# Performance work log

Measured on AMD Instinct MI355X. Metric: run time of the kernel, lower is better.

The kernel has to match this reference:

```python
import jax, jax.numpy as jnp
import numpy as np

BLOCK = 64
SCALING = 64 / 64  # alpha / block_size


def setup_inputs() -> dict:
    key = jax.random.key(0)
    ks = jax.random.split(key, 5)
    B, N, DIN, DOUT = 2, 2048, 4096, 4096
    nb_in, nb_out = DIN // BLOCK, DOUT // BLOCK
    return {
        "x": jax.random.normal(ks[0], (B, N, DIN), dtype=jnp.float32),
        "W_base": jax.random.normal(ks[1], (DOUT, DIN), dtype=jnp.float32) * 0.02,
        "b_base": jax.random.normal(ks[2], (DOUT,), dtype=jnp.float32),
        "U": jax.random.normal(ks[3], (BLOCK, nb_in, nb_out), dtype=jnp.float32) / BLOCK,
        "V": jax.random.normal(ks[4], (nb_out, BLOCK, BLOCK), dtype=jnp.float32) * 0.02,
        "S": jnp.ones((1,), dtype=jnp.float32),
    }


def reference(x, W_base, b_base, U, V, S):
    B, N, DIN = x.shape
    DOUT = W_base.shape[0]
    nb_in = U.shape[1]  # in_features // block_size
    # base linear: y = x @ W^T + b
    result = jnp.einsum("bnd,od->bno", x, W_base) + b_base
    # block-structured adapter path
    xr = x.reshape(B, N, nb_in, BLOCK)            # [b, n, in_blocks, block]
    t = jnp.einsum("bnid,dio->bnod", xr, U)       # mix across input blocks per lane d
    t = jnp.einsum("bnod,ode->bnoe", t, V)        # mix within each output block
    scaling = SCALING * S[0]
    result = result + scaling * t.reshape(B, N, DOUT)
    return result
```

## Files before the change

kernel.cpp:

```cpp
#include <hip/hip_runtime.h>


typedef __attribute__((ext_vector_type(4))) float float4v;
typedef __attribute__((ext_vector_type(4))) int   int4v;
typedef __attribute__((ext_vector_type(2))) int   int2v;

#define K_TOT 4096
#define M_TOT 4096
#define N_TOT 4096

__global__ void trans_uv(const float* __restrict__ U, const float* __restrict__ V,
                         float* __restrict__ Ut, float* __restrict__ Vt) {
  int idx = blockIdx.x * 256 + threadIdx.x;
  if (idx < 262144) {
    int d = idx & 63, o = (idx >> 6) & 63, i = idx >> 12;
    Ut[idx] = U[(d * 64 + i) * 64 + o];
  } else {
    int j = idx - 262144;
    int d = j & 63, e = (j >> 6) & 63, o = j >> 12;
    Vt[j] = V[(o * 64 + d) * 64 + e];
  }
}

__global__ __launch_bounds__(512) void quant_rows(
    const float* __restrict__ W, const float* __restrict__ Ut,
    const float* __restrict__ Vt, const float* __restrict__ Sp,
    const float* __restrict__ X, char* __restrict__ Wq, char* __restrict__ Xq,
    float* __restrict__ sw, float* __restrict__ sx) {
  __shared__ float red[8];
  const int row = blockIdx.x;
  const int t = threadIdx.x;
  const int c0 = t << 3;
  const float s = Sp[0];
  float4v v0, v1;
  if (row < 4096) {
    const int o = row >> 6, e = row & 63;
    const int i = c0 >> 6, d0 = c0 & 63;
    const float4v wv0 = *(const float4v*)(W + (size_t)row * 4096 + c0);
    const float4v wv1 = *(const float4v*)(W + (size_t)row * 4096 + c0 + 4);
    const float4v u40 = *(const float4v*)(Ut + (i * 64 + o) * 64 + d0);
    const float4v u41 = *(const float4v*)(Ut + (i * 64 + o) * 64 + d0 + 4);
    const float4v v40 = *(const float4v*)(Vt + (o * 64 + e) * 64 + d0);
    const float4v v41 = *(const float4v*)(Vt + (o * 64 + e) * 64 + d0 + 4);
#pragma unroll
    for (int j = 0; j < 4; ++j) {
      v0[j] = wv0[j] + s * u40[j] * v40[j];
      v1[j] = wv1[j] + s * u41[j] * v41[j];
    }
  } else {
    v0 = *(const float4v*)(X + (size_t)(row - 4096) * 4096 + c0);
    v1 = *(const float4v*)(X + (size_t)(row - 4096) * 4096 + c0 + 4);
  }
  float m = fmaxf(fmaxf(fmaxf(fabsf(v0[0]), fabsf(v0[1])),
                        fmaxf(fabsf(v0[2]), fabsf(v0[3]))),
                  fmaxf(fmaxf(fabsf(v1[0]), fabsf(v1[1])),
                        fmaxf(fabsf(v1[2]), fabsf(v1[3]))));
#pragma unroll
  for (int off = 32; off; off >>= 1) m = fmaxf(m, __shfl_xor(m, off));
  if ((t & 63) == 0) red[t >> 6] = m;
  __syncthreads();
  float mx = red[0];
#pragma unroll
  for (int r = 1; r < 8; ++r) mx = fmaxf(mx, red[r]);
  const float inv = mx > 0.f ? 127.f / mx : 0.f;
  int q[8];
#pragma unroll
  for (int j = 0; j < 4; ++j) {
    int a = __float2int_rn(v0[j] * inv);
    int b2 = __float2int_rn(v1[j] * inv);
    q[j] = a > 127 ? 127 : (a < -127 ? -127 : a);
    q[4 + j] = b2 > 127 ? 127 : (b2 < -127 ? -127 : b2);
  }
  int2v pk;
  pk[0] = (q[0] & 0xff) | ((q[1] & 0xff) << 8) | ((q[2] & 0xff) << 16) |
          (q[3] << 24);
  pk[1] = (q[4] & 0xff) | ((q[5] & 0xff) << 8) | ((q[6] & 0xff) << 16) |
          (q[7] << 24);
  if (row < 4096) {
    *(int2v*)(Wq + (size_t)row * 4096 + c0) = pk;
    if (t == 0) sw[row] = mx * (1.f / 127.f);
  } else {
    *(int2v*)(Xq + (size_t)(row - 4096) * 4096 + c0) = pk;
    if (t == 0) sx[row - 4096] = mx * (1.f / 127.f);
  }
}

#define GL16(g, l)                                                    \
  __builtin_amdgcn_global_load_lds(                                   \
      (__attribute__((address_space(1))) void*)(g),                   \
      (__attribute__((address_space(3))) void*)(l), 16, 0, 0)

#define BARRIER() asm volatile("s_barrier" ::: "memory")
#define VMC6() asm volatile("s_waitcnt vmcnt(6)" ::: "memory")
#define VMC0() asm volatile("s_waitcnt vmcnt(0)" ::: "memory")
#define VMNONE()

__global__ __launch_bounds__(512, 2) void gemm256(
    const char* __restrict__ A,
    const char* __restrict__ Bq,
    const float* __restrict__ bias,
    const float* __restrict__ sx,
    const float* __restrict__ sw,
    float* __restrict__ C) {
  __shared__ char lds[2][2][2][16384];

  const int tid = threadIdx.x;
  const int w = tid >> 6;
  const int l = tid & 63;
  const int l15 = l & 15;
  const int hi = l >> 4;

  int b = blockIdx.x;
  b = (b & 7) * 32 + (b >> 3);
  const int brow = (b >> 4) * 256;
  const int bcol = (b & 15) * 256;

  const int wr = w >> 2;
  const int wc = w & 3;
  const int wcH = wc >> 1, wcL = wc & 1;

  const int b2 = (l15 >> 2) & 1;
  const int cx = hi ^ (l15 & 3);
  const int rdK0 = (((b2 ^ 0) << 2) | cx) << 4;
  const int rdK1 = (((b2 ^ 1) << 2) | cx) << 4;
  const int rowOff = l15 << 7;

  const int rowL = l >> 3;
  const int cL = (l & 7) ^ rowL;
  const char* pa = A + (size_t)(brow + w * 8 + rowL) * 4096 + cL * 16;
  const char* pb = Bq + (size_t)(bcol + w * 8 + rowL) * 4096 + cL * 16;
  const int ldsC0 = w * 1024;
  const int ldsC1 = 8192 + w * 1024;

#define STAGE(gp, BUF, OP, H, kt)                                           \
  do {                                                                      \
    GL16((gp) + (size_t)(H) * (128 * 4096) + (kt), &lds[BUF][OP][H][ldsC0]);\
    GL16((gp) + (size_t)(H) * (128 * 4096) + (64 * 4096) + (kt),            \
         &lds[BUF][OP][H][ldsC1]);                                          \
  } while (0)

  int4v acc[8][4];
#pragma unroll
  for (int m = 0; m < 8; ++m)
#pragma unroll
    for (int j = 0; j < 4; ++j) acc[m][j] = (int4v){0, 0, 0, 0};
  int4v af[4][2];
  int4v bfr[4][2];

#define READ_A(BUF, MB)                                                     \
  _Pragma("unroll") for (int mm = 0; mm < 4; ++mm) {                        \
    const char* ap = &lds[BUF][0][wr][((MB) + mm) * 2048 + rowOff];         \
    af[mm][0] = *(const int4v*)&ap[rdK0];                                   \
    af[mm][1] = *(const int4v*)&ap[rdK1];                                   \
  }

#define READ_B(BUF, NH)                                                     \
  _Pragma("unroll") for (int jj = 0; jj < 2; ++jj) {                        \
    const char* bp =                                                        \
        &lds[BUF][1][wcH][((wcL)*64 + (NH)*32 + jj * 16) * 128 + rowOff];   \
    bfr[(NH)*2 + jj][0] = *(const int4v*)&bp[rdK0];                         \
    bfr[(NH)*2 + jj][1] = *(const int4v*)&bp[rdK1];                         \
  }

#define MFMA16(MB, NB)                                                      \
  do {                                                                      \
    __builtin_amdgcn_s_setprio(1);                                          \
    _Pragma("unroll") for (int mm = 0; mm < 4; ++mm)                        \
        _Pragma("unroll") for (int nn = 0; nn < 2; ++nn) {                  \
      acc[(MB) + mm][(NB) + nn] = __builtin_amdgcn_mfma_i32_16x16x64_i8(    \
          af[mm][0], bfr[(NB) + nn][0], acc[(MB) + mm][(NB) + nn], 0, 0, 0);\
      acc[(MB) + mm][(NB) + nn] = __builtin_amdgcn_mfma_i32_16x16x64_i8(    \
          af[mm][1], bfr[(NB) + nn][1], acc[(MB) + mm][(NB) + nn], 0, 0, 0);\
    }                                                                       \
    __builtin_amdgcn_s_setprio(0);                                          \
  } while (0)

#define TILE(BUF, TT, DA1, DB, DA0, VM)                                    \
  do {                                                                     \
    READ_A(BUF, 0); READ_B(BUF, 0);                                        \
    if (DA1) STAGE(pa, 1 - (BUF), 0, 1, ((TT) + 1) * 128);                 \
    BARRIER(); MFMA16(0, 0);                                               \
    READ_B(BUF, 1);                                                        \
    BARRIER(); MFMA16(0, 2);                                               \
    READ_A(BUF, 4);                                                        \
    if (DB) STAGE(pb, BUF, 1, 0, ((TT) + 2) * 128);                        \
    BARRIER(); MFMA16(4, 0);                                               \
    if (DB) STAGE(pb, BUF, 1, 1, ((TT) + 2) * 128);                        \
    if (DA0) STAGE(pa, BUF, 0, 0, ((TT) + 2) * 128);                       \
    VM();                                                                  \
    BARRIER(); MFMA16(4, 2);                                               \
  } while (0)

  STAGE(pa, 0, 0, 0, 0);
  STAGE(pa, 0, 0, 1, 0);
  STAGE(pb, 0, 1, 0, 0);
  STAGE(pb, 0, 1, 1, 0);
  STAGE(pb, 1, 1, 0, 128);
  STAGE(pb, 1, 1, 1, 128);
  STAGE(pa, 1, 0, 0, 128);
  VMC6();
  BARRIER();

  for (int t = 0; t < 30; t += 2) {
    TILE(0, t, 1, 1, 1, VMC6);
    TILE(1, t + 1, 1, 1, 1, VMC6);
  }
  TILE(0, 30, 1, 0, 0, VMC0);
  TILE(1, 31, 0, 0, 0, VMNONE);

  const int r0 = brow + wr * 128 + (l >> 4) * 4;
  const int c0 = bcol + wc * 64;
  float sxr[8][4];
#pragma unroll
  for (int m = 0; m < 8; ++m)
#pragma unroll
    for (int v = 0; v < 4; ++v) sxr[m][v] = sx[r0 + m * 16 + v];
#pragma unroll
  for (int j = 0; j < 4; ++j) {
    const int col = c0 + j * 16 + l15;
    const float bv = bias[col];
    const float swc = sw[col];
#pragma unroll
    for (int m = 0; m < 8; ++m) {
      const int row = r0 + m * 16;
#pragma unroll
      for (int v = 0; v < 4; ++v)
        C[(size_t)(row + v) * N_TOT + col] =
            (float)acc[m][j][v] * (sxr[m][v] * swc) + bv;
    }
  }
}

extern "C" void kernel_launch(void* const* d_in, const int* in_sizes, int n_in,
                              void* d_out, int out_size, void* d_ws, size_t ws_size,
                              hipStream_t stream) {
  const float* x = (const float*)d_in[0];
  const float* Wb = (const float*)d_in[1];
  const float* bb = (const float*)d_in[2];
  const float* U = (const float*)d_in[3];
  const float* V = (const float*)d_in[4];
  const float* S = (const float*)d_in[5];
  float* out = (float*)d_out;

  char* Wq = (char*)d_ws;
  char* Xq = Wq + (size_t)4096 * 4096;
  float* sw = (float*)(Xq + (size_t)4096 * 4096);
  float* sx = sw + 4096;
  float* Ut = (float*)d_out;
  float* Vt = Ut + 262144;

  trans_uv<<<2048, 256, 0, stream>>>(U, V, Ut, Vt);
  quant_rows<<<8192, 512, 0, stream>>>(Wb, Ut, Vt, S, x, Wq, Xq, sw, sx);

  gemm256<<<256, 512, 0, stream>>>(Xq, Wq, bb, sx, sw, out);
}
```

Measured before the change: 96.16 us.

## Use 4 waves per block with 128x128 warp tiles and simpler double-buffer schedule

Shrinks the GEMM block from 8 waves to 4, so each wave computes a 128x128 tile with 8x8 accumulators. Each wave now issues four global-to-LDS loads per stage. The interleaved stage/barrier/MFMA pipeline is replaced by a simpler per-tile flow: wait, barrier, read all fragments, run all MFMAs, barrier, then issue the next loads. The goal is more fragment reuse per LDS read and fewer barriers, at the cost of much higher register pressure, fewer waves per CU, and less overlap of loads with compute.

```diff
diff --git a/kernel.cpp b/kernel.cpp
--- a/kernel.cpp
+++ b/kernel.cpp
@@ -91,11 +91,10 @@
       (__attribute__((address_space(3))) void*)(l), 16, 0, 0)
 
 #define BARRIER() asm volatile("s_barrier" ::: "memory")
-#define VMC6() asm volatile("s_waitcnt vmcnt(6)" ::: "memory")
+#define VMC16() asm volatile("s_waitcnt vmcnt(16)" ::: "memory")
 #define VMC0() asm volatile("s_waitcnt vmcnt(0)" ::: "memory")
-#define VMNONE()
-
-__global__ __launch_bounds__(512, 2) void gemm256(
+
+__global__ __launch_bounds__(256, 1) void gemm256(
     const char* __restrict__ A,
     const char* __restrict__ Bq,
     const float* __restrict__ bias,
@@ -115,9 +114,8 @@
   const int brow = (b >> 4) * 256;
   const int bcol = (b & 15) * 256;
 
-  const int wr = w >> 2;
-  const int wc = w & 3;
-  const int wcH = wc >> 1, wcL = wc & 1;
+  const int wr = w >> 1;
+  const int wc = w & 1;
 
   const int b2 = (l15 >> 2) & 1;
   const int cx = hi ^ (l15 & 3);
@@ -129,94 +127,99 @@
   const int cL = (l & 7) ^ rowL;
   const char* pa = A + (size_t)(brow + w * 8 + rowL) * 4096 + cL * 16;
   const char* pb = Bq + (size_t)(bcol + w * 8 + rowL) * 4096 + cL * 16;
-  const int ldsC0 = w * 1024;
-  const int ldsC1 = 8192 + w * 1024;
-
-#define STAGE(gp, BUF, OP, H, kt)                                           \
-  do {                                                                      \
-    GL16((gp) + (size_t)(H) * (128 * 4096) + (kt), &lds[BUF][OP][H][ldsC0]);\
-    GL16((gp) + (size_t)(H) * (128 * 4096) + (64 * 4096) + (kt),            \
-         &lds[BUF][OP][H][ldsC1]);                                          \
+  const int ldsW = w * 1024;
+
+#define STAGE(gp, BUF, OP, H, kt)                                             \
+  do {                                                                        \
+    GL16((gp) + (size_t)(H) * (128 * 4096) + (kt),                            \
+         &lds[BUF][OP][H][ldsW]);                                             \
+    GL16((gp) + (size_t)(H) * (128 * 4096) + (32 * 4096) + (kt),              \
+         &lds[BUF][OP][H][4096 + ldsW]);                                      \
+    GL16((gp) + (size_t)(H) * (128 * 4096) + (64 * 4096) + (kt),              \
+         &lds[BUF][OP][H][8192 + ldsW]);                                      \
+    GL16((gp) + (size_t)(H) * (128 * 4096) + (96 * 4096) + (kt),              \
+         &lds[BUF][OP][H][12288 + ldsW]);                                     \
   } while (0)
 
-  int4v acc[8][4];
+  int4v acc[8][8];
 #pragma unroll
   for (int m = 0; m < 8; ++m)
 #pragma unroll
-    for (int j = 0; j < 4; ++j) acc[m][j] = (int4v){0, 0, 0, 0};
-  int4v af[4][2];
-  int4v bfr[4][2];
+    for (int j = 0; j < 8; ++j) acc[m][j] = (int4v){0, 0, 0, 0};
+  int4v af[8][2];
+  int4v bfr[8][2];
 
 #define READ_A(BUF, MB)                                                     \
   _Pragma("unroll") for (int mm = 0; mm < 4; ++mm) {                        \
     const char* ap = &lds[BUF][0][wr][((MB) + mm) * 2048 + rowOff];         \
-    af[mm][0] = *(const int4v*)&ap[rdK0];                                   \
-    af[mm][1] = *(const int4v*)&ap[rdK1];                                   \
-  }
-
-#define READ_B(BUF, NH)                                                     \
-  _Pragma("unroll") for (int jj = 0; jj < 2; ++jj) {                        \
-    const char* bp =                                                        \
-        &lds[BUF][1][wcH][((wcL)*64 + (NH)*32 + jj * 16) * 128 + rowOff];   \
-    bfr[(NH)*2 + jj][0] = *(const int4v*)&bp[rdK0];                         \
-    bfr[(NH)*2 + jj][1] = *(const int4v*)&bp[rdK1];                         \
-  }
-
-#define MFMA16(MB, NB)                                                      \
-  do {                                                                      \
-    __builtin_amdgcn_s_setprio(1);                                          \
-    _Pragma("unroll") for (int mm = 0; mm < 4; ++mm)                        \
-        _Pragma("unroll") for (int nn = 0; nn < 2; ++nn) {                  \
-      acc[(MB) + mm][(NB) + nn] = __builtin_amdgcn_mfma_i32_16x16x64_i8(    \
-          af[mm][0], bfr[(NB) + nn][0], acc[(MB) + mm][(NB) + nn], 0, 0, 0);\
-      acc[(MB) + mm][(NB) + nn] = __builtin_amdgcn_mfma_i32_16x16x64_i8(    \
-          af[mm][1], bfr[(NB) + nn][1], acc[(MB) + mm][(NB) + nn], 0, 0, 0);\
-    }                                                                       \
-    __builtin_amdgcn_s_setprio(0);                                          \
-  } while (0)
-
-#define TILE(BUF, TT, DA1, DB, DA0, VM)                                    \
+    af[(MB) + mm][0] = *(const int4v*)&ap[rdK0];                            \
+    af[(MB) + mm][1] = *(const int4v*)&ap[rdK1];                            \
+  }
+
+#define READ_B(BUF, NB)                                                     \
+  _Pragma("unroll") for (int jj = 0; jj < 4; ++jj) {                        \
+    const char* bp = &lds[BUF][1][wc][((NB) + jj) * 2048 + rowOff];         \
+    bfr[(NB) + jj][0] = *(const int4v*)&bp[rdK0];                           \
+    bfr[(NB) + jj][1] = *(const int4v*)&bp[rdK1];                           \
+  }
+
+#define MFMA32(MB, NB)                                                      \
+  _Pragma("unroll") for (int mm = 0; mm < 4; ++mm)                          \
+      _Pragma("unroll") for (int nn = 0; nn < 4; ++nn) {                    \
+    acc[(MB) + mm][(NB) + nn] = __builtin_amdgcn_mfma_i32_16x16x64_i8(      \
+        af[(MB) + mm][0], bfr[(NB) + nn][0], acc[(MB) + mm][(NB) + nn],     \
+        0, 0, 0);                                                           \
+    acc[(MB) + mm][(NB) + nn] = __builtin_amdgcn_mfma_i32_16x16x64_i8(      \
+        af[(MB) + mm][1], bfr[(NB) + nn][1], acc[(MB) + mm][(NB) + nn],     \
+        0, 0, 0);                                                           \
+  }
+
+#define TILE(BUF, TT, DOS, VM)                                             \
   do {                                                                     \
-    READ_A(BUF, 0); READ_B(BUF, 0);                                        \
-    if (DA1) STAGE(pa, 1 - (BUF), 0, 1, ((TT) + 1) * 128);                 \
-    BARRIER(); MFMA16(0, 0);                                               \
-    READ_B(BUF, 1);                                                        \
-    BARRIER(); MFMA16(0, 2);                                               \
+    VM();                                                                  \
+    BARRIER();                                                             \
+    READ_A(BUF, 0);                                                        \
+    READ_B(BUF, 0);                                                        \
     READ_A(BUF, 4);                                                        \
-    if (DB) STAGE(pb, BUF, 1, 0, ((TT) + 2) * 128);                        \
-    BARRIER(); MFMA16(4, 0);                                               \
-    if (DB) STAGE(pb, BUF, 1, 1, ((TT) + 2) * 128);                        \
-    if (DA0) STAGE(pa, BUF, 0, 0, ((TT) + 2) * 128);                       \
-    VM();                                                                  \
-    BARRIER(); MFMA16(4, 2);                                               \
+    READ_B(BUF, 4);                                                        \
+    MFMA32(0, 0);                      \
+    MFMA32(4, 0);                                             \
+    MFMA32(0, 4);                                    \
+    MFMA32(4, 4);                                                          \
+    BARRIER();                                                             \
+    if (DOS) {                                                             \
+      STAGE(pa, BUF, 0, 0, ((TT) + 2) * 128);                              \
+      STAGE(pa, BUF, 0, 1, ((TT) + 2) * 128);                              \
+      STAGE(pb, BUF, 1, 0, ((TT) + 2) * 128);                              \
+      STAGE(pb, BUF, 1, 1, ((TT) + 2) * 128);                              \
+    }                                                                      \
   } while (0)
 
   STAGE(pa, 0, 0, 0, 0);
   STAGE(pa, 0, 0, 1, 0);
   STAGE(pb, 0, 1, 0, 0);
   STAGE(pb, 0, 1, 1, 0);
+  STAGE(pa, 1, 0, 0, 128);
+  STAGE(pa, 1, 0, 1, 128);
   STAGE(pb, 1, 1, 0, 128);
   STAGE(pb, 1, 1, 1, 128);
-  STAGE(pa, 1, 0, 0, 128);
-  VMC6();
-  BARRIER();
 
   for (int t = 0; t < 30; t += 2) {
-    TILE(0, t, 1, 1, 1, VMC6);
-    TILE(1, t + 1, 1, 1, 1, VMC6);
-  }
-  TILE(0, 30, 1, 0, 0, VMC0);
-  TILE(1, 31, 0, 0, 0, VMNONE);
+    TILE(0, t, 1, VMC16);
+    TILE(1, t + 1, 1, VMC16);
+  }
+  TILE(0, 30, 0, VMC16);
+  TILE(1, 31, 0, VMC0);
 
   const int r0 = brow + wr * 128 + (l >> 4) * 4;
-  const int c0 = bcol + wc * 64;
+  const int c0 = bcol + wc * 128;
   float sxr[8][4];
 #pragma unroll
   for (int m = 0; m < 8; ++m)
 #pragma unroll
     for (int v = 0; v < 4; ++v) sxr[m][v] = sx[r0 + m * 16 + v];
 #pragma unroll
-  for (int j = 0; j < 4; ++j) {
+  for (int j = 0; j < 8; ++j) {
     const int col = c0 + j * 16 + l15;
     const float bv = bias[col];
     const float swc = sw[col];
@@ -252,5 +255,5 @@
   trans_uv<<<2048, 256, 0, stream>>>(U, V, Ut, Vt);
   quant_rows<<<8192, 512, 0, stream>>>(Wb, Ut, Vt, S, x, Wq, Xq, sw, sx);
 
-  gemm256<<<256, 512, 0, stream>>>(Xq, Wq, bb, sx, sw, out);
-}
+  gemm256<<<256, 256, 0, stream>>>(Xq, Wq, bb, sx, sw, out);
+}
```

Result: slower. 109.3 us (+13.6%).
